# Kernel tuning notes

Hardware: AMD Instinct MI355X
Metric: run time of the kernel (lower is better)

The kernel has to match this reference:

```python
import jax, jax.numpy as jnp
import numpy as np

N_NODES = 8192
N_EDGES = 32768
D = 768
H1 = 8
NEG_SLOPE = 0.2


def setup_inputs() -> dict:
    key = jax.random.key(0)
    ks = jax.random.split(key, 10)
    s = 0.02  # init scale keeps attention logits numerically tame
    x = jax.random.normal(ks[0], (N_NODES, D), dtype=jnp.float32)
    edge_index = jax.random.randint(ks[1], (2, N_EDGES), 0, N_NODES, dtype=jnp.int64)
    W1 = jax.random.normal(ks[2], (D, H1 * D), dtype=jnp.float32) * s
    a_src1 = jax.random.normal(ks[3], (H1, D), dtype=jnp.float32) * s
    a_dst1 = jax.random.normal(ks[4], (H1, D), dtype=jnp.float32) * s
    b1 = jnp.zeros((H1 * D,), dtype=jnp.float32)
    W2 = jax.random.normal(ks[5], (H1 * D, D), dtype=jnp.float32) * s
    a_src2 = jax.random.normal(ks[6], (1, D), dtype=jnp.float32) * s
    a_dst2 = jax.random.normal(ks[7], (1, D), dtype=jnp.float32) * s
    b2 = jnp.zeros((D,), dtype=jnp.float32)
    return {"x": x, "edge_index": edge_index, "W1": W1, "a_src1": a_src1,
            "a_dst1": a_dst1, "b1": b1, "W2": W2, "a_src2": a_src2,
            "a_dst2": a_dst2, "b2": b2}


def gat_conv(x, src, dst, W, a_src, a_dst, b, heads, out_ch):
    """PyG GATConv (concat=True, self-loops already appended to src/dst)."""
    n = x.shape[0]
    h = (x @ W).reshape(n, heads, out_ch)            # [N,H,C]
    alpha_src = jnp.einsum("nhc,hc->nh", h, a_src)  # [N,H]
    alpha_dst = jnp.einsum("nhc,hc->nh", h, a_dst)  # [N,H]
    # edge scores: leaky_relu(a_src.h_j + a_dst.h_i) for edge j->i
    e = jax.nn.leaky_relu(alpha_src[src] + alpha_dst[dst], NEG_SLOPE)  # [E,H]
    # segment softmax over incoming edges of each destination node
    m = jax.ops.segment_max(e, dst, num_segments=n)   # [N,H]
    m = jnp.where(jnp.isfinite(m), m, 0.0)
    p = jnp.exp(e - m[dst])                           # [E,H]
    denom = jax.ops.segment_sum(p, dst, num_segments=n)
    alpha = p / denom[dst]                            # [E,H]
    msg = h[src] * alpha[:, :, None]                  # [E,H,C] gather+weight
    out = jax.ops.segment_sum(msg, dst, num_segments=n)  # [N,H,C] scatter-add
    return out.reshape(n, heads * out_ch) + b


def reference(x, edge_index, W1, a_src1, a_dst1, b1, W2, a_src2, a_dst2, b2):
    n = x.shape[0]
    loops = jnp.arange(n, dtype=edge_index.dtype)
    src = jnp.concatenate([edge_index[0], loops])  # add_self_loops=True
    dst = jnp.concatenate([edge_index[1], loops])
    h = gat_conv(x, src, dst, W1, a_src1, a_dst1, b1, H1, D)
    h = jax.nn.elu(h)
    out = gat_conv(h, src, dst, W2, a_src2, a_dst2, b2, 1, D)
    return out
```

## Files before the change

kernel.cpp:

```cpp
#include <hip/hip_runtime.h>
#include <hip/hip_bf16.h>


#define N_NODES 8192
#define N_EDGES 32768
#define E_TOT   (N_EDGES + N_NODES)
#define D_IN    768
#define H1      8
#define HC1     (H1 * D_IN)
#define KSPLIT  4
#define KSLICE  (HC1 / KSPLIT)

typedef unsigned short ushort_t;
using short8  = __attribute__((ext_vector_type(8))) short;
using floatx4 = __attribute__((ext_vector_type(4))) float;

__device__ __forceinline__ float bf2f(unsigned short u) {
  return __uint_as_float(((unsigned)u) << 16);
}
__device__ __forceinline__ unsigned short f2bf(float f) {
  unsigned u = __float_as_uint(f);
  unsigned r = (u + 0x7fffu + ((u >> 16) & 1u)) >> 16;
  return (unsigned short)r;
}

__device__ __forceinline__ void gll16(const ushort_t* g, ushort_t* l) {
  __builtin_amdgcn_global_load_lds(
      (const __attribute__((address_space(1))) void*)g,
      (__attribute__((address_space(3))) void*)l, 16, 0, 0);
}

__global__ __launch_bounds__(64) void frag_transpose_kernel(
    const float* __restrict__ W, ushort_t* __restrict__ out,
    int Kdim, int Ndim) {
  const int bn = blockIdx.x;
  const int bk = blockIdx.y;
  const int lane = threadIdx.x;
  const int lrow = lane & 15, lq = lane >> 4;
  const int n = bn * 16 + lrow;
  const int kb = bk * 32 + lq * 8;
  ushort_t v[8];
#pragma unroll
  for (int e = 0; e < 8; ++e)
    v[e] = f2bf(W[(size_t)(kb + e) * Ndim + n]);
  *(short8*)(out + ((size_t)bn * (Kdim >> 5) + bk) * 512 + lane * 8) =
      *(short8*)v;
}

__global__ void prep_aw_kernel(const float* __restrict__ W1,
                               const float* __restrict__ aS,
                               const float* __restrict__ aD,
                               float* __restrict__ awS,
                               float* __restrict__ awD) {
  const int d = blockIdx.x;
  const int t = threadIdx.x;
  const float* row = W1 + (size_t)d * HC1;
  float ps[H1], pd[H1];
#pragma unroll
  for (int h = 0; h < H1; ++h) { ps[h] = 0.f; pd[h] = 0.f; }
#pragma unroll
  for (int h = 0; h < H1; ++h)
#pragma unroll
    for (int j = 0; j < 3; ++j) {
      int idx = h * 768 + j * 256 + t;
      float w = row[idx];
      ps[h] += w * aS[idx];
      pd[h] += w * aD[idx];
    }
#pragma unroll
  for (int h = 0; h < H1; ++h)
    for (int off = 32; off > 0; off >>= 1) {
      ps[h] += __shfl_down(ps[h], off, 64);
      pd[h] += __shfl_down(pd[h], off, 64);
    }
  __shared__ float red[2][4][H1];
  int w = t >> 6;
  if ((t & 63) == 0) {
#pragma unroll
    for (int h = 0; h < H1; ++h) { red[0][w][h] = ps[h]; red[1][w][h] = pd[h]; }
  }
  __syncthreads();
  if (t < H1)
    awS[d * H1 + t] = red[0][0][t] + red[0][1][t] + red[0][2][t] + red[0][3][t];
  else if (t >= 64 && t < 64 + H1) {
    int h = t - 64;
    awD[d * H1 + h] = red[1][0][h] + red[1][1][h] + red[1][2][h] + red[1][3][h];
  }
}

__global__ void node_prep_kernel(const float* __restrict__ x,
                                 const float* __restrict__ awS,
                                 const float* __restrict__ awD,
                                 ushort_t* __restrict__ xb,
                                 float* __restrict__ as1,
                                 float* __restrict__ ad1) {
  const int n = blockIdx.x;
  const int t = threadIdx.x;
  float ps[H1], pd[H1];
#pragma unroll
  for (int h = 0; h < H1; ++h) { ps[h] = 0.f; pd[h] = 0.f; }
#pragma unroll
  for (int j = 0; j < 3; ++j) {
    int d = j * 256 + t;
    float xv = x[(size_t)n * 768 + d];
    xb[(size_t)n * 768 + d] = f2bf(xv);
    const float4* s4 = (const float4*)(awS + d * 8);
    const float4* d4 = (const float4*)(awD + d * 8);
    float4 a0 = s4[0], a1 = s4[1];
    float4 c0 = d4[0], c1 = d4[1];
    ps[0] += xv * a0.x; ps[1] += xv * a0.y; ps[2] += xv * a0.z; ps[3] += xv * a0.w;
    ps[4] += xv * a1.x; ps[5] += xv * a1.y; ps[6] += xv * a1.z; ps[7] += xv * a1.w;
    pd[0] += xv * c0.x; pd[1] += xv * c0.y; pd[2] += xv * c0.z; pd[3] += xv * c0.w;
    pd[4] += xv * c1.x; pd[5] += xv * c1.y; pd[6] += xv * c1.z; pd[7] += xv * c1.w;
  }
#pragma unroll
  for (int h = 0; h < H1; ++h)
    for (int off = 32; off > 0; off >>= 1) {
      ps[h] += __shfl_down(ps[h], off, 64);
      pd[h] += __shfl_down(pd[h], off, 64);
    }
  __shared__ float red[2][4][H1];
  int w = t >> 6;
  if ((t & 63) == 0) {
#pragma unroll
    for (int h = 0; h < H1; ++h) { red[0][w][h] = ps[h]; red[1][w][h] = pd[h]; }
  }
  __syncthreads();
  if (t < H1)
    as1[n * H1 + t] = red[0][0][t] + red[0][1][t] + red[0][2][t] + red[0][3][t];
  else if (t >= 64 && t < 64 + H1) {
    int h = t - 64;
    ad1[n * H1 + h] = red[1][0][h] + red[1][1][h] + red[1][2][h] + red[1][3][h];
  }
}

__global__ void deg_kernel(const int* __restrict__ dst, int* __restrict__ deg) {
  int e = blockIdx.x * blockDim.x + threadIdx.x;
  if (e >= E_TOT) return;
  int d = (e < N_EDGES) ? dst[e] : (e - N_EDGES);
  atomicAdd(&deg[d], 1);
}

__global__ void scan_kernel(const int* __restrict__ deg, int* __restrict__ start,
                            int* __restrict__ cursor) {
  __shared__ int sums[1024];
  int t = threadIdx.x;
  int base = t * 8;
  int local[8];
  int s = 0;
#pragma unroll
  for (int i = 0; i < 8; ++i) { local[i] = s; s += deg[base + i]; }
  sums[t] = s;
  __syncthreads();
  for (int off = 1; off < 1024; off <<= 1) {
    int v = (t >= off) ? sums[t - off] : 0;
    __syncthreads();
    sums[t] += v;
    __syncthreads();
  }
  int excl = (t == 0) ? 0 : sums[t - 1];
#pragma unroll
  for (int i = 0; i < 8; ++i) {
    int st = excl + local[i];
    start[base + i] = st;
    cursor[base + i] = st;
  }
}

__global__ void fill_kernel(const int* __restrict__ dst, int* __restrict__ cursor,
                            int* __restrict__ csr) {
  int e = blockIdx.x * blockDim.x + threadIdx.x;
  if (e >= E_TOT) return;
  int d = (e < N_EDGES) ? dst[e] : (e - N_EDGES);
  int pos = atomicAdd(&cursor[d], 1);
  csr[pos] = e;
}

__global__ __launch_bounds__(256) void attn1_kernel(
    const ushort_t* __restrict__ xb, const float* __restrict__ as1,
    const float* __restrict__ ad1, const int* __restrict__ start,
    const int* __restrict__ deg, const int* __restrict__ csr,
    const int* __restrict__ src, ushort_t* __restrict__ z_sw) {
  const int n = blockIdx.x;
  const int t = threadIdx.x;
  const int st = start[n], dg = deg[n];
  const int h = t & 7, eloc = t >> 3;
  __shared__ float invd[H1];
  __shared__ float alphaS[32][H1];
  __shared__ int sidx[32];
  __shared__ float red[4][H1];

  const float adv = ad1[n * H1 + h];
  float pden = 0.f;
  for (int base = 0; base < dg; base += 32) {
    int ei = base + eloc;
    if (ei < dg) {
      int e = csr[st + ei];
      int s = (e < N_EDGES) ? src[e] : (e - N_EDGES);
      float l = as1[s * H1 + h] + adv;
      l = l > 0.f ? l : 0.2f * l;
      pden += __expf(l);
    }
  }
  pden += __shfl_down(pden, 8, 64);
  pden += __shfl_down(pden, 16, 64);
  pden += __shfl_down(pden, 32, 64);
  if ((t & 63) < 8) red[t >> 6][h] = pden;
  __syncthreads();
  if (t < 8) invd[t] = 1.0f / (red[0][t] + red[1][t] + red[2][t] + red[3][t]);
  __syncthreads();

  int hp[3], ip[3];
#pragma unroll
  for (int p = 0; p < 3; ++p) {
    int c8 = p * 256 + t;
    hp[p] = c8 / 96;
    ip[p] = c8 % 96;
  }
  float acc[3][8];
#pragma unroll
  for (int p = 0; p < 3; ++p)
#pragma unroll
    for (int e = 0; e < 8; ++e) acc[p][e] = 0.f;

  for (int base = 0; base < dg; base += 32) {
    int cnt = dg - base; if (cnt > 32) cnt = 32;
    if (eloc < cnt) {
      int e = csr[st + base + eloc];
      int s = (e < N_EDGES) ? src[e] : (e - N_EDGES);
      float l = as1[s * H1 + h] + adv;
      l = l > 0.f ? l : 0.2f * l;
      alphaS[eloc][h] = __expf(l) * invd[h];
      if (h == 0) sidx[eloc] = s;
    }
    __syncthreads();
    for (int ei = 0; ei < cnt; ++ei) {
      int s = sidx[ei];
      const uint4* xrow = (const uint4*)(xb + (size_t)s * 768);
#pragma unroll
      for (int p = 0; p < 3; ++p) {
        uint4 v = xrow[ip[p]];
        float al = alphaS[ei][hp[p]];
        unsigned uu[4] = {v.x, v.y, v.z, v.w};
#pragma unroll
        for (int q = 0; q < 4; ++q) {
          acc[p][2 * q]     += al * __uint_as_float(uu[q] << 16);
          acc[p][2 * q + 1] += al * __uint_as_float(uu[q] & 0xffff0000u);
        }
      }
    }
    __syncthreads();
  }
#pragma unroll
  for (int p = 0; p < 3; ++p) {
    int c8 = p * 256 + t;
    int k = c8 * 8;
    size_t chunk = (size_t)(n >> 4) * 192 + (k >> 5);
    int word = ((k >> 3) & 3) * 16 + (n & 15);
    ushort_t v[8];
#pragma unroll
    for (int e = 0; e < 8; ++e) v[e] = f2bf(acc[p][e]);
    *(short8*)(z_sw + chunk * 512 + word * 8) = *(short8*)v;
  }
}

#define STAGE_RING(t)                                                          \
  {                                                                            \
    ushort_t* ld_ = smem + ((t) & 3) * 16384 + slot512;                        \
    _Pragma("unroll") for (int q_ = 0; q_ < 4; ++q_)                           \
        gll16(SRC + (((size_t)(cb[q_] + (t))) << 9) + lane8, ld_ + q_ * 512);  \
  }

#define GSTEP_BODY(s, VMSTR, NSV)                                             \
  {                                                                           \
    asm volatile("s_waitcnt vmcnt(" VMSTR ")" ::: "memory");                  \
    __builtin_amdgcn_s_barrier();                                             \
    if ((s) + 3 < (NSV)) STAGE_RING((s) + 3)                                  \
    const ushort_t* buf_ = smem + ((s) & 3) * 16384;                          \
    short8 af[8], bf[4];                                                      \
    _Pragma("unroll") for (int i_ = 0; i_ < 8; ++i_)                          \
        af[i_] = *(const short8*)(buf_ + (wm * 8 + i_) * 512 + lane8);        \
    _Pragma("unroll") for (int j_ = 0; j_ < 4; ++j_)                          \
        bf[j_] = *(const short8*)(buf_ + 8192 + (wn * 4 + j_) * 512 + lane8); \
    __builtin_amdgcn_s_setprio(1);                                            \
    _Pragma("unroll") for (int i_ = 0; i_ < 8; ++i_)                          \
        _Pragma("unroll") for (int j_ = 0; j_ < 4; ++j_)                      \
            acc[i_][j_] = __builtin_amdgcn_mfma_f32_16x16x32_bf16(            \
                af[i_], bf[j_], acc[i_][j_], 0, 0, 0);                        \
    __builtin_amdgcn_s_setprio(0);                                            \
  }

#define GEMM_PIPE(NSV)                                                        \
  _Pragma("unroll") for (int p_ = 0; p_ < 3; ++p_) STAGE_RING(p_)             \
  _Pragma("unroll 4") for (int s_ = 0; s_ < (NSV)-2; ++s_) {                  \
    GSTEP_BODY(s_, "8", (NSV))                                                \
  }                                                                           \
  GSTEP_BODY((NSV)-2, "4", (NSV))                                             \
  GSTEP_BODY((NSV)-1, "0", (NSV))

__global__ __launch_bounds__(512, 2) void gemm_l1_kernel(
    const ushort_t* __restrict__ Asw, const ushort_t* __restrict__ Bsw,
    const float* __restrict__ biasb, ushort_t* __restrict__ Csw) {
  __shared__ ushort_t smem[4 * 16384];
  const int id = blockIdx.x;
  const int head = id & 7;
  const int j_id = id >> 3;
  const int n_t = j_id % 3;
  const int m_t = j_id / 3;
  const int tid = threadIdx.x;
  const int lane = tid & 63;
  const int w = tid >> 6;
  const int wm = w >> 2, wn = w & 3;
  const int lrow = lane & 15, lq = lane >> 4;
  const int lane8 = lane * 8;
  const int slot512 = w * 2048;
  const ushort_t* SRC = (w < 4) ? Asw : Bsw;

  int cb[4];
#pragma unroll
  for (int q = 0; q < 4; ++q) {
    int v;
    if (w < 4)
      v = (m_t * 16 + 4 * w + q) * 192 + head * 24;
    else
      v = (head * 48 + n_t * 16 + 4 * (w - 4) + q) * 24;
    cb[q] = __builtin_amdgcn_readfirstlane(v);
  }

  floatx4 acc[8][4];
#pragma unroll
  for (int i = 0; i < 8; ++i)
#pragma unroll
    for (int j = 0; j < 4; ++j) acc[i][j] = {0.f, 0.f, 0.f, 0.f};

  GEMM_PIPE(24)

  ushort_t* tile = smem;
  const float* bias = biasb + head * 768 + n_t * 256;
#pragma unroll
  for (int p = 0; p < 2; ++p) {
    if (p) __syncthreads();
    if (wm == p) {
#pragma unroll
      for (int i = 0; i < 8; ++i)
#pragma unroll
        for (int j = 0; j < 4; ++j) {
          int col = wn * 64 + j * 16 + lrow;
          float bv = bias[col];
#pragma unroll
          for (int r = 0; r < 4; ++r) {
            float v = acc[i][j][r] + bv;
            v = v > 0.f ? v : __expf(v) - 1.0f;
            tile[(i * 16 + lq * 4 + r) * 280 + col] = f2bf(v);
          }
        }
    }
    __syncthreads();
#pragma unroll
    for (int cc = 0; cc < 8; ++cc) {
      int ch = w * 8 + cc;
      int RB = ch >> 3, kg = ch & 7;
      short8 vv =
          *(const short8*)&tile[(RB * 16 + lrow) * 280 + kg * 32 + lq * 8];
      size_t chunk_g = (size_t)(m_t * 16 + p * 8 + RB) * 192 + head * 24 +
                       n_t * 8 + kg;
      *((short8*)Csw + chunk_g * 64 + lane) = vv;
    }
  }
}

__global__ __launch_bounds__(512, 2) void gemm_l2_kernel(
    const ushort_t* __restrict__ Asw, const ushort_t* __restrict__ Bsw,
    float* __restrict__ Cp) {
  __shared__ ushort_t smem[4 * 16384];
  const int id = blockIdx.x;
  const int c = id & 7;
  const int sl = c >> 1;
  const int j_id = id >> 3;
  const int n_t = j_id % 3;
  const int m_t = (j_id / 3) * 2 + (c & 1);
  const int tid = threadIdx.x;
  const int lane = tid & 63;
  const int w = tid >> 6;
  const int wm = w >> 2, wn = w & 3;
  const int lrow = lane & 15, lq = lane >> 4;
  const int lane8 = lane * 8;
  const int slot512 = w * 2048;
  const ushort_t* SRC = (w < 4) ? Asw : Bsw;

  int cb[4];
#pragma unroll
  for (int q = 0; q < 4; ++q) {
    int v;
    if (w < 4)
      v = (m_t * 16 + 4 * w + q) * 192 + sl * 48;
    else
      v = (n_t * 16 + 4 * (w - 4) + q) * 192 + sl * 48;
    cb[q] = __builtin_amdgcn_readfirstlane(v);
  }

  floatx4 acc[8][4];
#pragma unroll
  for (int i = 0; i < 8; ++i)
#pragma unroll
    for (int j = 0; j < 4; ++j) acc[i][j] = {0.f, 0.f, 0.f, 0.f};

  GEMM_PIPE(48)

  float* C = Cp + (size_t)sl * N_NODES * 768;
  const int m0 = m_t * 256, n0 = n_t * 256;
#pragma unroll
  for (int i = 0; i < 8; ++i) {
    int row_b = m0 + wm * 128 + i * 16 + lq * 4;
#pragma unroll
    for (int j = 0; j < 4; ++j) {
      int col = n0 + wn * 64 + j * 16 + lrow;
#pragma unroll
      for (int r = 0; r < 4; ++r)
        C[(size_t)(row_b + r) * 768 + col] = acc[i][j][r];
    }
  }
}

__global__ void reduce_alpha2_kernel(const float* __restrict__ parts,
                                     const float* __restrict__ aS,
                                     const float* __restrict__ aD,
                                     ushort_t* __restrict__ yb,
                                     float* __restrict__ as2,
                                     float* __restrict__ ad2) {
  const int n = blockIdx.x;
  const int t = threadIdx.x;
  const size_t S = (size_t)N_NODES * 768;
  float ps = 0.f, pd = 0.f;
#pragma unroll
  for (int j = 0; j < 3; ++j) {
    int cidx = j * 256 + t;
    size_t base = (size_t)n * 768 + cidx;
    float v = parts[base] + parts[base + S] + parts[base + 2 * S] +
              parts[base + 3 * S];
    yb[base] = f2bf(v);
    ps += v * aS[cidx];
    pd += v * aD[cidx];
  }
  for (int off = 32; off > 0; off >>= 1) {
    ps += __shfl_down(ps, off, 64);
    pd += __shfl_down(pd, off, 64);
  }
  __shared__ float red[2][4];
  int w = t >> 6;
  if ((t & 63) == 0) { red[0][w] = ps; red[1][w] = pd; }
  __syncthreads();
  if (t == 0) as2[n] = red[0][0] + red[0][1] + red[0][2] + red[0][3];
  if (t == 64) ad2[n] = red[1][0] + red[1][1] + red[1][2] + red[1][3];
}

__global__ __launch_bounds__(256) void attn2_kernel(
    const ushort_t* __restrict__ yb, const float* __restrict__ as2,
    const float* __restrict__ ad2, const int* __restrict__ start,
    const int* __restrict__ deg, const int* __restrict__ csr,
    const int* __restrict__ src, const float* __restrict__ b2,
    float* __restrict__ out) {
  const int n = blockIdx.x;
  const int t = threadIdx.x;
  const int st = start[n], dg = deg[n];
  __shared__ float alphaS[64];
  __shared__ int sidx[64];
  __shared__ float red[4];
  __shared__ float invd_sh;

  const float adv = ad2[n];
  float pden = 0.f;
  for (int ei = t; ei < dg; ei += 256) {
    int e = csr[st + ei];
    int s = (e < N_EDGES) ? src[e] : (e - N_EDGES);
    float l = as2[s] + adv;
    l = l > 0.f ? l : 0.2f * l;
    pden += __expf(l);
  }
  for (int off = 32; off > 0; off >>= 1) pden += __shfl_down(pden, off, 64);
  if ((t & 63) == 0) red[t >> 6] = pden;
  __syncthreads();
  if (t == 0) invd_sh = 1.0f / (red[0] + red[1] + red[2] + red[3]);
  __syncthreads();
  const float invd = invd_sh;

  float a0 = 0.f, a1 = 0.f, a2 = 0.f;
  for (int base = 0; base < dg; base += 64) {
    int cnt = dg - base; if (cnt > 64) cnt = 64;
    if (t < cnt) {
      int e = csr[st + base + t];
      int s = (e < N_EDGES) ? src[e] : (e - N_EDGES);
      float l = as2[s] + adv;
      l = l > 0.f ? l : 0.2f * l;
      alphaS[t] = __expf(l) * invd;
      sidx[t] = s;
    }
    __syncthreads();
    for (int ei = 0; ei < cnt; ++ei) {
      float al = alphaS[ei];
      const ushort_t* row = yb + (size_t)sidx[ei] * 768;
      a0 += al * bf2f(row[t]);
      a1 += al * bf2f(row[t + 256]);
      a2 += al * bf2f(row[t + 512]);
    }
    __syncthreads();
  }
  out[(size_t)n * 768 + t]       = a0 + b2[t];
  out[(size_t)n * 768 + t + 256] = a1 + b2[t + 256];
  out[(size_t)n * 768 + t + 512] = a2 + b2[t + 512];
}

extern "C" void kernel_launch(void* const* d_in, const int* in_sizes, int n_in,
                              void* d_out, int out_size, void* d_ws, size_t ws_size,
                              hipStream_t stream) {
  const float* x      = (const float*)d_in[0];
  const int*   ei     = (const int*)d_in[1];
  const float* W1     = (const float*)d_in[2];
  const float* a_src1 = (const float*)d_in[3];
  const float* a_dst1 = (const float*)d_in[4];
  const float* b1     = (const float*)d_in[5];
  const float* W2     = (const float*)d_in[6];
  const float* a_src2 = (const float*)d_in[7];
  const float* a_dst2 = (const float*)d_in[8];
  const float* b2     = (const float*)d_in[9];
  float* out = (float*)d_out;
  const int* src = ei;
  const int* dst = ei + N_EDGES;

  char* ws = (char*)d_ws;
  size_t off = 0;
  auto alloc = [&](size_t bytes) -> void* {
    void* p = ws + off;
    off = (off + bytes + 255) & ~(size_t)255;
    return p;
  };

  int* deg = (int*)alloc(N_NODES * 4);
  float* awS = (float*)alloc(768 * H1 * 4);
  float* awD = (float*)alloc(768 * H1 * 4);
  float* as1 = (float*)alloc(N_NODES * H1 * 4);
  float* ad1 = (float*)alloc(N_NODES * H1 * 4);
  float* as2 = (float*)alloc(N_NODES * 4);
  float* ad2 = (float*)alloc(N_NODES * 4);
  int* start  = (int*)alloc(N_NODES * 4);
  int* cursor = (int*)alloc(N_NODES * 4);
  int* csr    = (int*)alloc(E_TOT * 4);
  ushort_t* xb     = (ushort_t*)alloc((size_t)N_NODES * D_IN * 2);
  ushort_t* w1t_sw = (ushort_t*)alloc((size_t)HC1 * D_IN * 2 + 8192);
  ushort_t* w2t_sw = (ushort_t*)alloc((size_t)HC1 * D_IN * 2 + 8192);
  ushort_t* z_sw   = (ushort_t*)alloc((size_t)N_NODES * HC1 * 2 + 8192);
  ushort_t* h2b_sw = (ushort_t*)alloc((size_t)N_NODES * HC1 * 2 + 8192);
  ushort_t* yb  = xb;
  float* parts  = (float*)z_sw;
  (void)ws_size; (void)n_in; (void)in_sizes; (void)out_size;

  hipMemsetAsync(deg, 0, N_NODES * 4, stream);

  prep_aw_kernel<<<768, 256, 0, stream>>>(W1, a_src1, a_dst1, awS, awD);
  node_prep_kernel<<<N_NODES, 256, 0, stream>>>(x, awS, awD, xb, as1, ad1);
  frag_transpose_kernel<<<dim3(HC1 / 16, D_IN / 32), 64, 0, stream>>>(
      W1, w1t_sw, D_IN, HC1);
  frag_transpose_kernel<<<dim3(D_IN / 16, HC1 / 32), 64, 0, stream>>>(
      W2, w2t_sw, HC1, D_IN);

  deg_kernel<<<(E_TOT + 255) / 256, 256, 0, stream>>>(dst, deg);
  scan_kernel<<<1, 1024, 0, stream>>>(deg, start, cursor);
  fill_kernel<<<(E_TOT + 255) / 256, 256, 0, stream>>>(dst, cursor, csr);

  attn1_kernel<<<N_NODES, 256, 0, stream>>>(xb, as1, ad1, start, deg, csr,
                                            src, z_sw);
  gemm_l1_kernel<<<8 * 32 * 3, 512, 0, stream>>>(z_sw, w1t_sw, b1, h2b_sw);

  gemm_l2_kernel<<<KSPLIT * 2 * 16 * 3, 512, 0, stream>>>(h2b_sw, w2t_sw,
                                                          parts);
  reduce_alpha2_kernel<<<N_NODES, 256, 0, stream>>>(parts, a_src2, a_dst2, yb,
                                                    as2, ad2);
  attn2_kernel<<<N_NODES, 256, 0, stream>>>(yb, as2, ad2, start, deg, csr,
                                            src, b2, out);
}
```

Baseline: 462.4 us.

## Restructure GEMM pipeline into double-buffered 64-K steps with half-step staging

Replaces the 4-slot ring of 32-wide K stages with a 2-slot double buffer of 64-wide K steps, each split into two halves. The next step's half is staged just before the matching half is computed. This halves the loop trip count and changes the wait and barrier pattern, aiming to cut loop overhead and keep prefetch overlap. It adds a __syncthreads before the L1 epilogue reuses shared memory. The risk is shorter prefetch lead time, which could expose load latency.

```diff
diff --git a/kernel.cpp b/kernel.cpp
--- a/kernel.cpp
+++ b/kernel.cpp
@@ -264,24 +264,22 @@
   }
 }
 
-#define STAGE_RING(t)                                                          \
-  {                                                                            \
-    ushort_t* ld_ = smem + ((t) & 3) * 16384 + slot512;                        \
-    _Pragma("unroll") for (int q_ = 0; q_ < 4; ++q_)                           \
-        gll16(SRC + (((size_t)(cb[q_] + (t))) << 9) + lane8, ld_ + q_ * 512);  \
-  }
-
-#define GSTEP_BODY(s, VMSTR, NSV)                                             \
+#define STAGE_HALF(t, kk)                                                     \
   {                                                                           \
-    asm volatile("s_waitcnt vmcnt(" VMSTR ")" ::: "memory");                  \
-    __builtin_amdgcn_s_barrier();                                             \
-    if ((s) + 3 < (NSV)) STAGE_RING((s) + 3)                                  \
-    const ushort_t* buf_ = smem + ((s) & 3) * 16384;                          \
+    ushort_t* ld_ = smem + ((t) & 1) * 32768 + (kk) * 16384 + slotu;          \
+    _Pragma("unroll") for (int q_ = 0; q_ < 4; ++q_)                          \
+        gll16(SRC + (((size_t)(cb[q_] + 2 * (t) + (kk))) << 9) + lane8,       \
+              ld_ + q_ * 512);                                                \
+  }
+
+#define HALF_COMPUTE(s, kk)                                                   \
+  {                                                                           \
+    const ushort_t* hb_ = smem + ((s) & 1) * 32768 + (kk) * 16384;            \
     short8 af[8], bf[4];                                                      \
+    _Pragma("unroll") for (int j_ = 0; j_ < 4; ++j_)                          \
+        bf[j_] = *(const short8*)(hb_ + 8192 + (wn * 4 + j_) * 512 + lane8);  \
     _Pragma("unroll") for (int i_ = 0; i_ < 8; ++i_)                          \
-        af[i_] = *(const short8*)(buf_ + (wm * 8 + i_) * 512 + lane8);        \
-    _Pragma("unroll") for (int j_ = 0; j_ < 4; ++j_)                          \
-        bf[j_] = *(const short8*)(buf_ + 8192 + (wn * 4 + j_) * 512 + lane8); \
+        af[i_] = *(const short8*)(hb_ + (wm * 8 + i_) * 512 + lane8);         \
     __builtin_amdgcn_s_setprio(1);                                            \
     _Pragma("unroll") for (int i_ = 0; i_ < 8; ++i_)                          \
         _Pragma("unroll") for (int j_ = 0; j_ < 4; ++j_)                      \
@@ -290,18 +288,29 @@
     __builtin_amdgcn_s_setprio(0);                                            \
   }
 
-#define GEMM_PIPE(NSV)                                                        \
-  _Pragma("unroll") for (int p_ = 0; p_ < 3; ++p_) STAGE_RING(p_)             \
-  _Pragma("unroll 4") for (int s_ = 0; s_ < (NSV)-2; ++s_) {                  \
-    GSTEP_BODY(s_, "8", (NSV))                                                \
+#define GSTEP64(s, VMT, VMM, NSV)                                             \
+  {                                                                           \
+    asm volatile("s_waitcnt vmcnt(" VMT ")" ::: "memory");                    \
+    __builtin_amdgcn_s_barrier();                                             \
+    if ((s) + 1 < (NSV)) STAGE_HALF((s) + 1, 0)                               \
+    HALF_COMPUTE(s, 0)                                                        \
+    asm volatile("s_waitcnt vmcnt(" VMM ")" ::: "memory");                    \
+    __builtin_amdgcn_s_barrier();                                             \
+    if ((s) + 1 < (NSV)) STAGE_HALF((s) + 1, 1)                               \
+    HALF_COMPUTE(s, 1)                                                        \
+  }
+
+#define GEMM_PIPE64(NSV)                                                      \
+  STAGE_HALF(0, 0) STAGE_HALF(0, 1)                                           \
+  _Pragma("unroll 2") for (int s_ = 0; s_ < (NSV)-1; ++s_) {                  \
+    GSTEP64(s_, "4", "4", (NSV))                                              \
   }                                                                           \
-  GSTEP_BODY((NSV)-2, "4", (NSV))                                             \
-  GSTEP_BODY((NSV)-1, "0", (NSV))
+  GSTEP64((NSV)-1, "4", "0", (NSV))
 
 __global__ __launch_bounds__(512, 2) void gemm_l1_kernel(
     const ushort_t* __restrict__ Asw, const ushort_t* __restrict__ Bsw,
     const float* __restrict__ biasb, ushort_t* __restrict__ Csw) {
-  __shared__ ushort_t smem[4 * 16384];
+  __shared__ ushort_t smem[65536];
   const int id = blockIdx.x;
   const int head = id & 7;
   const int j_id = id >> 3;
@@ -313,7 +322,7 @@
   const int wm = w >> 2, wn = w & 3;
   const int lrow = lane & 15, lq = lane >> 4;
   const int lane8 = lane * 8;
-  const int slot512 = w * 2048;
+  const int slotu = (w < 4) ? w * 2048 : 8192 + (w - 4) * 2048;
   const ushort_t* SRC = (w < 4) ? Asw : Bsw;
 
   int cb[4];
@@ -333,8 +342,9 @@
 #pragma unroll
     for (int j = 0; j < 4; ++j) acc[i][j] = {0.f, 0.f, 0.f, 0.f};
 
-  GEMM_PIPE(24)
-
+  GEMM_PIPE64(12)
+
+  __syncthreads();
   ushort_t* tile = smem;
   const float* bias = biasb + head * 768 + n_t * 256;
 #pragma unroll
@@ -372,7 +382,7 @@
 __global__ __launch_bounds__(512, 2) void gemm_l2_kernel(
     const ushort_t* __restrict__ Asw, const ushort_t* __restrict__ Bsw,
     float* __restrict__ Cp) {
-  __shared__ ushort_t smem[4 * 16384];
+  __shared__ ushort_t smem[65536];
   const int id = blockIdx.x;
   const int c = id & 7;
   const int sl = c >> 1;
@@ -385,7 +395,7 @@
   const int wm = w >> 2, wn = w & 3;
   const int lrow = lane & 15, lq = lane >> 4;
   const int lane8 = lane * 8;
-  const int slot512 = w * 2048;
+  const int slotu = (w < 4) ? w * 2048 : 8192 + (w - 4) * 2048;
   const ushort_t* SRC = (w < 4) ? Asw : Bsw;
 
   int cb[4];
@@ -405,7 +415,7 @@
 #pragma unroll
     for (int j = 0; j < 4; ++j) acc[i][j] = {0.f, 0.f, 0.f, 0.f};
 
-  GEMM_PIPE(48)
+  GEMM_PIPE64(24)
 
   float* C = Cp + (size_t)sl * N_NODES * 768;
   const int m0 = m_t * 256, n0 = n_t * 256;
```

Result: slower. 487.7 us (+5.5%).
